# Performance work log

Hardware: AMD Instinct MI355X
Metric: run time of the kernel (lower is better)

Reference implementation:

```python
import jax, jax.numpy as jnp
import numpy as np

B, N, E = 2, 2048, 1024
H = 16
D = E // H  # head dim = 64


def setup_inputs() -> dict:
    key = jax.random.key(0)
    ks = jax.random.split(key, 11)
    s = 1.0 / np.sqrt(E)
    return {
        "q": jax.random.normal(ks[0], (B, N, E), jnp.float32),
        "k": jax.random.normal(ks[1], (B, N, E), jnp.float32),
        "v": jax.random.normal(ks[2], (B, N, E), jnp.float32),
        "Wq": jax.random.normal(ks[3], (E, E), jnp.float32) * s,
        "bq": jnp.zeros((E,), jnp.float32),
        "Wk": jax.random.normal(ks[4], (E, E), jnp.float32) * s,
        "bk": jnp.zeros((E,), jnp.float32),
        "Wv": jax.random.normal(ks[5], (E, E), jnp.float32) * s,
        "bv": jnp.zeros((E,), jnp.float32),
        "Wo": jax.random.normal(ks[6], (E, E), jnp.float32) * s,
        "bo": jnp.zeros((E,), jnp.float32),
    }


def reference(q, k, v, Wq, bq, Wk, bk, Wv, bv, Wo, bo):
    # projections (torch Linear: x @ W^T + b)
    qp = q @ Wq.T + bq  # [B,N,E]
    kp = k @ Wk.T + bk
    vp = v @ Wv.T + bv
    # separate heads -> [B,H,N,D]
    qh = qp.reshape(B, N, H, D).transpose(0, 2, 1, 3)
    kh = kp.reshape(B, N, H, D).transpose(0, 2, 1, 3)
    vh = vp.reshape(B, N, H, D).transpose(0, 2, 1, 3)
    # scaled dot-product attention, full score matrix like the original
    scale = 1.0 / jnp.sqrt(jnp.asarray(D, qh.dtype))
    attn = jnp.einsum('bhqd,bhkd->bhqk', qh, kh) * scale
    attn = jax.nn.softmax(attn, axis=-1)
    out = jnp.einsum('bhqk,bhkd->bhqd', attn, vh)  # [B,H,N,D]
    # recombine heads
    out = out.transpose(0, 2, 1, 3).reshape(B, N, E)
    return out @ Wo.T + bo
```

## Files before the change

kernel.cpp:

```cpp
#include <hip/hip_runtime.h>

typedef _Float16 f16;
typedef __attribute__((ext_vector_type(2))) _Float16 f16x2;
typedef __attribute__((ext_vector_type(4))) _Float16 f16x4;
typedef __attribute__((ext_vector_type(8))) _Float16 f16x8;
typedef __attribute__((ext_vector_type(4))) float    f32x4;
typedef __attribute__((ext_vector_type(16))) float   f32x16;
typedef __attribute__((ext_vector_type(4))) unsigned u32x4;

static constexpr int B_ = 2, N_ = 2048, E_ = 1024, H_ = 16, D_ = 64;

#define MFMA16(a, b, c) __builtin_amdgcn_mfma_f32_16x16x32_f16(a, b, c, 0, 0, 0)
#define MFMA32(a, b, c) __builtin_amdgcn_mfma_f32_32x32x16_f16(a, b, c, 0, 0, 0)

#define QSCALE 0.18033688011112042f

__global__ __launch_bounds__(256) void castw_kernel(
    const float* __restrict__ Wq, const float* __restrict__ Wk,
    const float* __restrict__ Wv, const float* __restrict__ Wo,
    f16* __restrict__ dst)
{
    const int i = (blockIdx.x * 256 + threadIdx.x) * 4;
    const int which = i >> 20;
    const float* s = (which == 0) ? Wq : (which == 1) ? Wk : (which == 2) ? Wv : Wo;
    const int j = i & (E_ * E_ - 1);
    const f32x4 f = *(const f32x4*)&s[j];
    f16x4 o;
    o[0] = (f16)f[0]; o[1] = (f16)f[1]; o[2] = (f16)f[2]; o[3] = (f16)f[3];
    *(f16x4*)&dst[i] = o;
}

__global__ __launch_bounds__(256) void proj_gemm(
    const float* __restrict__ q, const float* __restrict__ k, const float* __restrict__ v,
    const f16* __restrict__ Wb,
    const float* __restrict__ bq, const float* __restrict__ bk, const float* __restrict__ bv,
    f16* __restrict__ qh, f16* __restrict__ kh, f16* __restrict__ vt)
{
    const int z = blockIdx.z;
    const float* A    = (z == 0) ? q  : (z == 1) ? k  : v;
    const f16*   W    = Wb + (size_t)z * E_ * E_;
    const float* bias = (z == 0) ? bq : (z == 1) ? bk : bv;

    __shared__ f16 As[128][40];
    __shared__ f16 Bs[128][40];

    const int tid  = threadIdx.x;
    const int lane = tid & 63, w = tid >> 6;
    const int lr = lane & 15, lg = lane >> 4;
    const int wm = (w >> 1) * 64, wn = (w & 1) * 64;
    const int m0 = blockIdx.y * 128, n0 = blockIdx.x * 128;

    const int srow = tid >> 1;
    const int skh  = (tid & 1) * 16;

    f32x4 acc[4][4];
#pragma unroll
    for (int i = 0; i < 4; i++)
#pragma unroll
        for (int j = 0; j < 4; j++) acc[i][j] = (f32x4){0.f, 0.f, 0.f, 0.f};

    for (int k0 = 0; k0 < E_; k0 += 32) {
        __syncthreads();
        {
            const float* src = &A[(size_t)(m0 + srow) * E_ + k0 + skh];
            const f32x4 f0 = *(const f32x4*)(src + 0);
            const f32x4 f1 = *(const f32x4*)(src + 4);
            const f32x4 f2 = *(const f32x4*)(src + 8);
            const f32x4 f3 = *(const f32x4*)(src + 12);
            f16x8 b0, b1;
#pragma unroll
            for (int t = 0; t < 4; t++) { b0[t] = (f16)f0[t]; b0[4 + t] = (f16)f1[t]; }
#pragma unroll
            for (int t = 0; t < 4; t++) { b1[t] = (f16)f2[t]; b1[4 + t] = (f16)f3[t]; }
            *(f16x8*)&As[srow][skh]     = b0;
            *(f16x8*)&As[srow][skh + 8] = b1;
        }
        {
            const f16* src = &W[(size_t)(n0 + srow) * E_ + k0 + skh];
            *(f16x8*)&Bs[srow][skh]     = *(const f16x8*)(src);
            *(f16x8*)&Bs[srow][skh + 8] = *(const f16x8*)(src + 8);
        }
        __syncthreads();

        f16x8 af[4], bfr[4];
#pragma unroll
        for (int ms = 0; ms < 4; ms++) af[ms]  = *(const f16x8*)&As[wm + ms * 16 + lr][lg * 8];
#pragma unroll
        for (int ns = 0; ns < 4; ns++) bfr[ns] = *(const f16x8*)&Bs[wn + ns * 16 + lr][lg * 8];
#pragma unroll
        for (int ms = 0; ms < 4; ms++)
#pragma unroll
            for (int ns = 0; ns < 4; ns++)
                acc[ms][ns] = MFMA16(af[ms], bfr[ns], acc[ms][ns]);
    }

    const float oscale = (z == 0) ? QSCALE : 1.0f;
#pragma unroll
    for (int ms = 0; ms < 4; ms++) {
        const int mbase = m0 + wm + ms * 16 + lg * 4;
#pragma unroll
        for (int ns = 0; ns < 4; ns++) {
            const int n  = n0 + wn + ns * 16 + lr;
            const float bn = bias[n];
            const int hh = n >> 6, dd = n & 63;
#pragma unroll
            for (int r = 0; r < 4; r++) {
                const float val = (acc[ms][ns][r] + bn) * oscale;
                const int mm = mbase + r;
                const int bb = mm >> 11;
                const int nn = mm & (N_ - 1);
                if (z == 2) {
                    vt[((size_t)(bb * H_ + hh) * D_ + dd) * N_ + nn] = (f16)val;
                } else {
                    f16* dst = (z == 0) ? qh : kh;
                    dst[((size_t)(bb * H_ + hh) * N_ + nn) * D_ + dd] = (f16)val;
                }
            }
        }
    }
}

__global__ __launch_bounds__(256) void attn_kernel(
    const f16* __restrict__ qh, const f16* __restrict__ kh,
    const f16* __restrict__ vt, f16* __restrict__ ao)
{
    const int bid = blockIdx.x;
    const int swz = (bid & 7) * 64 + (bid >> 3);
    const int qt = swz & 15;
    const int bh = swz >> 4;

    const int tid = threadIdx.x;
    const int w = tid >> 6, lane = tid & 63;
    const int l31 = lane & 31;
    const bool hi = (lane >> 5) != 0;
    const int hib = hi ? 1 : 0;

    const f16* qp = qh + (size_t)bh * N_ * D_;
    const f16* kp = kh + (size_t)bh * N_ * D_;
    const f16* vp = vt + (size_t)bh * D_ * N_;

    const int qrow = qt * 128 + w * 32 + l31;

    f16x8 qf[4];
#pragma unroll
    for (int ks = 0; ks < 4; ks++)
        qf[ks] = *(const f16x8*)&qp[(size_t)qrow * D_ + ks * 16 + hib * 8];

    __shared__ f16 Ks[2][64][64];
    __shared__ f16 Vs[2][64][64];

    const int srow = tid >> 3;
    const int sch  = tid & 7;
    const int ssl  = (sch ^ (srow & 7)) * 8;

    const f16* kg0 = kp + (size_t)srow * D_ + sch * 8;
    const f16* kg1 = kg0 + (size_t)32 * D_;
    const f16* vg0 = vp + (size_t)srow * N_ + sch * 8;
    const f16* vg1 = vg0 + (size_t)32 * N_;

    f32x16 oT0 = {0.f,0.f,0.f,0.f,0.f,0.f,0.f,0.f,0.f,0.f,0.f,0.f,0.f,0.f,0.f,0.f};
    f32x16 oT1 = oT0;
    float mrun = -3.0e38f, lrun = 0.f;

    f16x8 kr0 = *(const f16x8*)(kg0);
    f16x8 kr1 = *(const f16x8*)(kg1);
    f16x8 vr0 = *(const f16x8*)(vg0);
    f16x8 vr1 = *(const f16x8*)(vg1);

    constexpr int NT = N_ / 64;
    int cur = 0;

    for (int t = 0; t < NT; ++t) {
        *(f16x8*)&Ks[cur][srow     ][ssl] = kr0;
        *(f16x8*)&Ks[cur][srow + 32][ssl] = kr1;
        *(f16x8*)&Vs[cur][srow     ][ssl] = vr0;
        *(f16x8*)&Vs[cur][srow + 32][ssl] = vr1;
        if (t + 1 < NT) {
            kr0 = *(const f16x8*)(kg0 + (size_t)(t + 1) * 64 * D_);
            kr1 = *(const f16x8*)(kg1 + (size_t)(t + 1) * 64 * D_);
            vr0 = *(const f16x8*)(vg0 + (t + 1) * 64);
            vr1 = *(const f16x8*)(vg1 + (t + 1) * 64);
        }
        __syncthreads();

        f32x16 sA = {0.f,0.f,0.f,0.f,0.f,0.f,0.f,0.f,0.f,0.f,0.f,0.f,0.f,0.f,0.f,0.f};
        f32x16 sB = sA;
        __builtin_amdgcn_s_setprio(1);
#pragma unroll
        for (int ks = 0; ks < 4; ks++) {
            const int c = (ks * 2 + hib) ^ (l31 & 7);
            const f16x8 kfA = *(const f16x8*)&Ks[cur][l31     ][c * 8];
            const f16x8 kfB = *(const f16x8*)&Ks[cur][l31 + 32][c * 8];
            sA = MFMA32(kfA, qf[ks], sA);
            sB = MFMA32(kfB, qf[ks], sB);
        }
        __builtin_amdgcn_s_setprio(0);

        float tt[16];
#pragma unroll
        for (int r = 0; r < 16; r++) tt[r] = fmaxf(sA[r], sB[r]);
#pragma unroll
        for (int d = 8; d >= 1; d >>= 1)
#pragma unroll
            for (int r = 0; r < d; r++) tt[r] = fmaxf(tt[r], tt[r + d]);
        tt[0] = fmaxf(tt[0], __shfl_xor(tt[0], 32));
        const float mnew = fmaxf(mrun, tt[0]);
        const float alpha = __builtin_amdgcn_exp2f(mrun - mnew);
        mrun = mnew;
        float p0 = 0.f, p1 = 0.f, p2 = 0.f, p3 = 0.f;
#pragma unroll
        for (int r = 0; r < 16; r += 4) {
            sA[r]   = __builtin_amdgcn_exp2f(sA[r]   - mnew); p0 += sA[r];
            sA[r+1] = __builtin_amdgcn_exp2f(sA[r+1] - mnew); p1 += sA[r+1];
            sA[r+2] = __builtin_amdgcn_exp2f(sA[r+2] - mnew); p2 += sA[r+2];
            sA[r+3] = __builtin_amdgcn_exp2f(sA[r+3] - mnew); p3 += sA[r+3];
        }
#pragma unroll
        for (int r = 0; r < 16; r += 4) {
            sB[r]   = __builtin_amdgcn_exp2f(sB[r]   - mnew); p0 += sB[r];
            sB[r+1] = __builtin_amdgcn_exp2f(sB[r+1] - mnew); p1 += sB[r+1];
            sB[r+2] = __builtin_amdgcn_exp2f(sB[r+2] - mnew); p2 += sB[r+2];
            sB[r+3] = __builtin_amdgcn_exp2f(sB[r+3] - mnew); p3 += sB[r+3];
        }
        float lsum = (p0 + p1) + (p2 + p3);
        lsum += __shfl_xor(lsum, 32);
        lrun = lrun * alpha + lsum;
#pragma unroll
        for (int r = 0; r < 16; r++) { oT0[r] *= alpha; oT1[r] *= alpha; }

        __builtin_amdgcn_s_setprio(1);
#define PVSTEP(PP0,PP1,PP2,PP3,PP4,PP5,PP6,PP7, KSI)                                   \
        {                                                                              \
            const unsigned w0 = __builtin_bit_cast(unsigned, __builtin_amdgcn_cvt_pkrtz(PP0, PP1)); \
            const unsigned w1 = __builtin_bit_cast(unsigned, __builtin_amdgcn_cvt_pkrtz(PP2, PP3)); \
            const unsigned w2 = __builtin_bit_cast(unsigned, __builtin_amdgcn_cvt_pkrtz(PP4, PP5)); \
            const unsigned w3 = __builtin_bit_cast(unsigned, __builtin_amdgcn_cvt_pkrtz(PP6, PP7)); \
            const unsigned x0 = (unsigned)__shfl_xor((int)w0, 32);                     \
            const unsigned x1 = (unsigned)__shfl_xor((int)w1, 32);                     \
            const unsigned x2 = (unsigned)__shfl_xor((int)w2, 32);                     \
            const unsigned x3 = (unsigned)__shfl_xor((int)w3, 32);                     \
            u32x4 pw;                                                                  \
            pw[0] = hi ? x2 : w0;                                                      \
            pw[1] = hi ? x3 : w1;                                                      \
            pw[2] = hi ? w2 : x0;                                                      \
            pw[3] = hi ? w3 : x1;                                                      \
            const f16x8 pa = __builtin_bit_cast(f16x8, pw);                            \
            const int c = ((KSI) * 2 + hib) ^ (l31 & 7);                               \
            const f16x8 vf0 = *(const f16x8*)&Vs[cur][l31     ][c * 8];                \
            const f16x8 vf1 = *(const f16x8*)&Vs[cur][l31 + 32][c * 8];                \
            oT0 = MFMA32(vf0, pa, oT0);                                                \
            oT1 = MFMA32(vf1, pa, oT1);                                                \
        }
        PVSTEP(sA[0],sA[1],sA[2],sA[3],sA[4],sA[5],sA[6],sA[7], 0)
        PVSTEP(sA[8],sA[9],sA[10],sA[11],sA[12],sA[13],sA[14],sA[15], 1)
        PVSTEP(sB[0],sB[1],sB[2],sB[3],sB[4],sB[5],sB[6],sB[7], 2)
        PVSTEP(sB[8],sB[9],sB[10],sB[11],sB[12],sB[13],sB[14],sB[15], 3)
#undef PVSTEP
        __builtin_amdgcn_s_setprio(0);

        cur ^= 1;
    }

    const float inv = 1.0f / lrun;
    const int b = bh >> 4, h = bh & 15;
    f16* dst = ao + (size_t)(b * N_ + qrow) * E_ + h * 64 + hib * 4;
#pragma unroll
    for (int g = 0; g < 4; g++) {
        f16x4 o0, o1;
#pragma unroll
        for (int j = 0; j < 4; j++) {
            o0[j] = (f16)(oT0[g * 4 + j] * inv);
            o1[j] = (f16)(oT1[g * 4 + j] * inv);
        }
        *(f16x4*)&dst[8 * g]      = o0;
        *(f16x4*)&dst[8 * g + 32] = o1;
    }
}

__global__ __launch_bounds__(256) void out_gemm(
    const f16* __restrict__ ao, const f16* __restrict__ Wo,
    const float* __restrict__ bo, float* __restrict__ out)
{
    __shared__ f16 As[128][40];
    __shared__ f16 Bs[128][40];

    const int tid  = threadIdx.x;
    const int lane = tid & 63, w = tid >> 6;
    const int lr = lane & 15, lg = lane >> 4;
    const int wm = (w >> 1) * 64, wn = (w & 1) * 64;
    const int m0 = blockIdx.y * 128, n0 = blockIdx.x * 128;

    const int srow = tid >> 1;
    const int skh  = (tid & 1) * 16;

    f32x4 acc[4][4];
#pragma unroll
    for (int i = 0; i < 4; i++)
#pragma unroll
        for (int j = 0; j < 4; j++) acc[i][j] = (f32x4){0.f, 0.f, 0.f, 0.f};

    for (int k0 = 0; k0 < E_; k0 += 32) {
        __syncthreads();
        {
            const f16* src = &ao[(size_t)(m0 + srow) * E_ + k0 + skh];
            *(f16x8*)&As[srow][skh]     = *(const f16x8*)(src);
            *(f16x8*)&As[srow][skh + 8] = *(const f16x8*)(src + 8);
        }
        {
            const f16* src = &Wo[(size_t)(n0 + srow) * E_ + k0 + skh];
            *(f16x8*)&Bs[srow][skh]     = *(const f16x8*)(src);
            *(f16x8*)&Bs[srow][skh + 8] = *(const f16x8*)(src + 8);
        }
        __syncthreads();

        f16x8 af[4], bfr[4];
#pragma unroll
        for (int ms = 0; ms < 4; ms++) af[ms]  = *(const f16x8*)&As[wm + ms * 16 + lr][lg * 8];
#pragma unroll
        for (int ns = 0; ns < 4; ns++) bfr[ns] = *(const f16x8*)&Bs[wn + ns * 16 + lr][lg * 8];
#pragma unroll
        for (int ms = 0; ms < 4; ms++)
#pragma unroll
            for (int ns = 0; ns < 4; ns++)
                acc[ms][ns] = MFMA16(af[ms], bfr[ns], acc[ms][ns]);
    }

#pragma unroll
    for (int ms = 0; ms < 4; ms++) {
        const int mbase = m0 + wm + ms * 16 + lg * 4;
#pragma unroll
        for (int ns = 0; ns < 4; ns++) {
            const int n = n0 + wn + ns * 16 + lr;
            const float bn = bo[n];
#pragma unroll
            for (int r = 0; r < 4; r++) {
                out[(size_t)(mbase + r) * E_ + n] = acc[ms][ns][r] + bn;
            }
        }
    }
}

extern "C" void kernel_launch(void* const* d_in, const int* in_sizes, int n_in,
                              void* d_out, int out_size, void* d_ws, size_t ws_size,
                              hipStream_t stream) {
    const float* q  = (const float*)d_in[0];
    const float* k  = (const float*)d_in[1];
    const float* v  = (const float*)d_in[2];
    const float* Wq = (const float*)d_in[3];
    const float* bq = (const float*)d_in[4];
    const float* Wk = (const float*)d_in[5];
    const float* bk = (const float*)d_in[6];
    const float* Wv = (const float*)d_in[7];
    const float* bv = (const float*)d_in[8];
    const float* Wo = (const float*)d_in[9];
    const float* bo = (const float*)d_in[10];
    float* out = (float*)d_out;

    char* ws = (char*)d_ws;
    f16* Wb = (f16*)ws;
    f16* qh = (f16*)(ws + (size_t) 8 * 1024 * 1024);
    f16* kh = (f16*)(ws + (size_t)16 * 1024 * 1024);
    f16* vt = (f16*)(ws + (size_t)24 * 1024 * 1024);
    f16* ao = (f16*)(ws + (size_t)32 * 1024 * 1024);

    castw_kernel<<<4096, 256, 0, stream>>>(Wq, Wk, Wv, Wo, Wb);
    proj_gemm<<<dim3(8, 32, 3), 256, 0, stream>>>(q, k, v, Wb, bq, bk, bv, qh, kh, vt);
    attn_kernel<<<512, 256, 0, stream>>>(qh, kh, vt, ao);
    out_gemm<<<dim3(8, 32), 256, 0, stream>>>(ao, Wb + (size_t)3 * E_ * E_, bo, out);
}
```

Measured before the change: 169.4 us.

## Remap GEMM block indices per XCD and skip softmax rescale below a threshold

The projection and output GEMMs switch to 1D grids with a block-id remap. Consecutive blocks on the same XCD (blockIdx mod 8) then cover contiguous tiles, which should improve L2 reuse of A rows and weight tiles. Separately, the attention kernel now rescales the running output and sum only when some lane's new max exceeds the stored max by more than 8 (log2 units), skipping the alpha multiplies in most iterations. The lazy rescale keeps results exact as long as exponents stay bounded, but adds a wave-wide vote and a branch.

```diff
diff --git a/kernel.cpp b/kernel.cpp
--- a/kernel.cpp
+++ b/kernel.cpp
@@ -36,7 +36,13 @@
     const float* __restrict__ bq, const float* __restrict__ bk, const float* __restrict__ bv,
     f16* __restrict__ qh, f16* __restrict__ kh, f16* __restrict__ vt)
 {
-    const int z = blockIdx.z;
+    const int bid  = blockIdx.x;
+    const int lin  = (bid & 7) * 96 + (bid >> 3);
+    const int z    = lin >> 8;
+    const int rem  = lin & 255;
+    const int m0   = (rem >> 3) * 128;
+    const int n0   = (rem & 7) * 128;
+
     const float* A    = (z == 0) ? q  : (z == 1) ? k  : v;
     const f16*   W    = Wb + (size_t)z * E_ * E_;
     const float* bias = (z == 0) ? bq : (z == 1) ? bk : bv;
@@ -48,7 +54,6 @@
     const int lane = tid & 63, w = tid >> 6;
     const int lr = lane & 15, lg = lane >> 4;
     const int wm = (w >> 1) * 64, wn = (w & 1) * 64;
-    const int m0 = blockIdx.y * 128, n0 = blockIdx.x * 128;
 
     const int srow = tid >> 1;
     const int skh  = (tid & 1) * 16;
@@ -203,30 +208,35 @@
         for (int d = 8; d >= 1; d >>= 1)
 #pragma unroll
             for (int r = 0; r < d; r++) tt[r] = fmaxf(tt[r], tt[r + d]);
-        tt[0] = fmaxf(tt[0], __shfl_xor(tt[0], 32));
-        const float mnew = fmaxf(mrun, tt[0]);
-        const float alpha = __builtin_amdgcn_exp2f(mrun - mnew);
-        mrun = mnew;
+        float pmax = fmaxf(tt[0], __shfl_xor(tt[0], 32));
+
+        if (!__all(pmax - mrun <= 8.0f)) {
+            const float mnew = fmaxf(mrun, pmax);
+            const float alpha = __builtin_amdgcn_exp2f(mrun - mnew);
+            mrun = mnew;
+            lrun *= alpha;
+#pragma unroll
+            for (int r = 0; r < 16; r++) { oT0[r] *= alpha; oT1[r] *= alpha; }
+        }
+
         float p0 = 0.f, p1 = 0.f, p2 = 0.f, p3 = 0.f;
 #pragma unroll
         for (int r = 0; r < 16; r += 4) {
-            sA[r]   = __builtin_amdgcn_exp2f(sA[r]   - mnew); p0 += sA[r];
-            sA[r+1] = __builtin_amdgcn_exp2f(sA[r+1] - mnew); p1 += sA[r+1];
-            sA[r+2] = __builtin_amdgcn_exp2f(sA[r+2] - mnew); p2 += sA[r+2];
-            sA[r+3] = __builtin_amdgcn_exp2f(sA[r+3] - mnew); p3 += sA[r+3];
+            sA[r]   = __builtin_amdgcn_exp2f(sA[r]   - mrun); p0 += sA[r];
+            sA[r+1] = __builtin_amdgcn_exp2f(sA[r+1] - mrun); p1 += sA[r+1];
+            sA[r+2] = __builtin_amdgcn_exp2f(sA[r+2] - mrun); p2 += sA[r+2];
+            sA[r+3] = __builtin_amdgcn_exp2f(sA[r+3] - mrun); p3 += sA[r+3];
         }
 #pragma unroll
         for (int r = 0; r < 16; r += 4) {
-            sB[r]   = __builtin_amdgcn_exp2f(sB[r]   - mnew); p0 += sB[r];
-            sB[r+1] = __builtin_amdgcn_exp2f(sB[r+1] - mnew); p1 += sB[r+1];
-            sB[r+2] = __builtin_amdgcn_exp2f(sB[r+2] - mnew); p2 += sB[r+2];
-            sB[r+3] = __builtin_amdgcn_exp2f(sB[r+3] - mnew); p3 += sB[r+3];
+            sB[r]   = __builtin_amdgcn_exp2f(sB[r]   - mrun); p0 += sB[r];
+            sB[r+1] = __builtin_amdgcn_exp2f(sB[r+1] - mrun); p1 += sB[r+1];
+            sB[r+2] = __builtin_amdgcn_exp2f(sB[r+2] - mrun); p2 += sB[r+2];
+            sB[r+3] = __builtin_amdgcn_exp2f(sB[r+3] - mrun); p3 += sB[r+3];
         }
         float lsum = (p0 + p1) + (p2 + p3);
         lsum += __shfl_xor(lsum, 32);
-        lrun = lrun * alpha + lsum;
-#pragma unroll
-        for (int r = 0; r < 16; r++) { oT0[r] *= alpha; oT1[r] *= alpha; }
+        lrun += lsum;
 
         __builtin_amdgcn_s_setprio(1);
 #define PVSTEP(PP0,PP1,PP2,PP3,PP4,PP5,PP6,PP7, KSI)                                   \
@@ -284,11 +294,15 @@
     __shared__ f16 As[128][40];
     __shared__ f16 Bs[128][40];
 
+    const int bid = blockIdx.x;
+    const int lin = (bid & 7) * 32 + (bid >> 3);
+    const int m0  = (lin >> 3) * 128;
+    const int n0  = (lin & 7) * 128;
+
     const int tid  = threadIdx.x;
     const int lane = tid & 63, w = tid >> 6;
     const int lr = lane & 15, lg = lane >> 4;
     const int wm = (w >> 1) * 64, wn = (w & 1) * 64;
-    const int m0 = blockIdx.y * 128, n0 = blockIdx.x * 128;
 
     const int srow = tid >> 1;
     const int skh  = (tid & 1) * 16;
@@ -364,7 +378,7 @@
     f16* ao = (f16*)(ws + (size_t)32 * 1024 * 1024);
 
     castw_kernel<<<4096, 256, 0, stream>>>(Wq, Wk, Wv, Wo, Wb);
-    proj_gemm<<<dim3(8, 32, 3), 256, 0, stream>>>(q, k, v, Wb, bq, bk, bv, qh, kh, vt);
+    proj_gemm<<<768, 256, 0, stream>>>(q, k, v, Wb, bq, bk, bv, qh, kh, vt);
     attn_kernel<<<512, 256, 0, stream>>>(qh, kh, vt, ao);
-    out_gemm<<<dim3(8, 32), 256, 0, stream>>>(ao, Wb + (size_t)3 * E_ * E_, bo, out);
-}
+    out_gemm<<<256, 256, 0, stream>>>(ao, Wb + (size_t)3 * E_ * E_, bo, out);
+}
```

Result: faster. 155.0 us (-8.5%).
